# Performance work log

Measured on AMD Instinct MI355X. Metric: run time of the kernel, lower is better.

## Reference

```python
import jax, jax.numpy as jnp
import numpy as np

NEURON_CDECAY = 0.5
NEURON_VDECAY = 0.75
NEURON_VTH = 0.5
SPIKE_WINDOW = 0.5


@jax.custom_vjp
def pseudo_spike(v):
    return (v > NEURON_VTH).astype(v.dtype)

def _ps_fwd(v):
    return pseudo_spike(v), v

def _ps_bwd(v, g):
    return (g * (jnp.abs(v - NEURON_VTH) < SPIKE_WINDOW).astype(g.dtype),)

pseudo_spike.defvjp(_ps_fwd, _ps_bwd)


def setup_inputs() -> dict:
    key = jax.random.key(0)
    ks = jax.random.split(key, 6)
    B, S, T, H, A = 4096, 256, 50, 256, 2
    # NCP mask with fanout=256 over 256 targets selects every target -> dense.
    x = jax.random.uniform(ks[0], (B, S, T), dtype=jnp.float32)
    w1 = jax.random.normal(ks[1], (S, H), dtype=jnp.float32)
    w2 = jax.random.normal(ks[2], (H, H), dtype=jnp.float32)
    w3 = jax.random.normal(ks[3], (H, H), dtype=jnp.float32)
    w4 = jax.random.normal(ks[4], (H, A), dtype=jnp.float32)
    b1 = jnp.zeros((H,), jnp.float32)
    b2 = jnp.zeros((H,), jnp.float32)
    b3 = jnp.zeros((H,), jnp.float32)
    b4 = jnp.zeros((A,), jnp.float32)
    return {"x": x, "w1": w1, "b1": b1, "w2": w2, "b2": b2,
            "w3": w3, "b3": b3, "w4": w4, "b4": b4, "batch_size": B}


def _lif(pre, W, b, u, v, s):
    # torch: linear(pre, weight=W.t(), bias=b) == pre @ W + b  (W is [src, tgt])
    cur = u * NEURON_CDECAY + pre @ W + b
    volt = v * NEURON_VDECAY * (1.0 - s) + cur
    spk = pseudo_spike(volt)
    return cur, volt, spk


def reference(x, w1, b1, w2, b2, w3, b3, w4, b4, batch_size):
    B = x.shape[0]
    T = x.shape[2]
    H1, H2, H3, A = w1.shape[1], w2.shape[1], w3.shape[1], w4.shape[1]
    z = lambda d: jnp.zeros((B, d), x.dtype)
    carry0 = (z(H1), z(H1), z(H1), z(H2), z(H2), z(H2),
              z(H3), z(H3), z(H3), z(A), z(A), z(A))
    xt = jnp.transpose(x, (2, 0, 1))  # [T, B, S]

    def step(carry, inp):
        u1, v1, s1, u2, v2, s2, u3, v3, s3, u4, v4, s4 = carry
        u1, v1, s1 = _lif(inp, w1, b1, u1, v1, s1)
        u2, v2, s2 = _lif(s1, w2, b2, u2, v2, s2)
        u3, v3, s3 = _lif(s2, w3, b3, u3, v3, s3)
        u4, v4, s4 = _lif(s3, w4, b4, u4, v4, s4)
        return (u1, v1, s1, u2, v2, s2, u3, v3, s3, u4, v4, s4), s4

    _, s4_all = jax.lax.scan(step, carry0, xt)  # [T, B, A]
    fc4_sumspike = jnp.sum(s4_all, axis=0) / T
    # faithful to the source: out is divided by batch_window a second time
    out = fc4_sumspike / T
    return out
```

## Files before the change

### kernel.cpp

```cpp
#include <hip/hip_runtime.h>

typedef unsigned short u16;
typedef unsigned int u32;

#define B_N 4096
#define S_N 256
#define T_N 50
#define H_N 256

#define W1F 0
#define W2F 65536
#define W3F 131072
#define W4F 196608
#define B1F 197120
#define B2F 197376
#define B3F 197632
#define B4F 197888
#define CVT_N 197890
#define FLAGI 198656

__device__ __forceinline__ float bf2f(u16 h) { return __uint_as_float(((u32)h) << 16); }
__device__ __forceinline__ u16 f2bf(float f) {
  u32 x = __float_as_uint(f);
  return (u16)((x + 0x7fffu + ((x >> 16) & 1u)) >> 16);
}
__device__ __forceinline__ float ld_f(const void* p, size_t i, int isbf) {
  return isbf ? bf2f(((const u16*)p)[i]) : ((const float*)p)[i];
}

__global__ void detect_dtype(const u16* __restrict__ x, int* __restrict__ flag) {
  __shared__ int cnt[256];
  int c = 0;
  for (int i = threadIdx.x; i < 4096; i += 256) c += (x[2 * i] <= 0x3F80u) ? 1 : 0;
  cnt[threadIdx.x] = c;
  __syncthreads();
  if (threadIdx.x == 0) {
    int tot = 0;
    for (int i = 0; i < 256; i++) tot += cnt[i];
    flag[0] = (tot > 3000) ? 1 : 0;
  }
}

__global__ void convert_inputs(const void* w1, const void* w2, const void* w3,
                               const void* w4, const void* b1, const void* b2,
                               const void* b3, const void* b4, float* __restrict__ ws) {
  const int isbf = ((const int*)ws)[FLAGI];
  int i = blockIdx.x * 256 + threadIdx.x;
  if (i >= CVT_N) return;
  float v;
  if (i < 196608) {
    const void* src = (i < 65536) ? w1 : (i < 131072 ? w2 : w3);
    v = ld_f(src, (size_t)(i & 65535), isbf);
  } else if (i < 197120) v = ld_f(w4, (size_t)(i - W4F), isbf);
  else if (i < 197376) v = ld_f(b1, (size_t)(i - B1F), isbf);
  else if (i < 197632) v = ld_f(b2, (size_t)(i - B2F), isbf);
  else if (i < 197888) v = ld_f(b3, (size_t)(i - B3F), isbf);
  else v = ld_f(b4, (size_t)(i - B4F), isbf);
  ws[i] = v;
}

template <int OFF, int TN>
__device__ __forceinline__ void gemm_win(const float* __restrict__ Wc,
                                         const float (*__restrict__ A)[52],
                                         int rdf, float (&acc)[13][4]) {
  for (int s = 0; s < S_N; s++) {
    const float w0 = Wc[(s << 8) + 0];
    const float w1 = Wc[(s << 8) + 64];
    const float w2 = Wc[(s << 8) + 128];
    const float w3 = Wc[(s << 8) + 192];
    const float4* ar = (const float4*)(&A[s][rdf]);
    const float4 q0 = ar[0], q1 = ar[1], q2 = ar[2], q3 = ar[3];
    const float a[16] = {q0.x, q0.y, q0.z, q0.w, q1.x, q1.y, q1.z, q1.w,
                         q2.x, q2.y, q2.z, q2.w, q3.x, q3.y, q3.z, q3.w};
#pragma unroll
    for (int i = 0; i < TN; i++) {
      acc[i][0] = fmaf(a[OFF + i], w0, acc[i][0]);
      acc[i][1] = fmaf(a[OFF + i], w1, acc[i][1]);
      acc[i][2] = fmaf(a[OFF + i], w2, acc[i][2]);
      acc[i][3] = fmaf(a[OFF + i], w3, acc[i][3]);
    }
  }
}

__global__ __launch_bounds__(256, 3) void snn_f32(
    const void* __restrict__ x, const float* __restrict__ ws, void* __restrict__ out) {
  __shared__ float Af[S_N][52];
  __shared__ float z4[T_N][2];

  const int b = blockIdx.x;
  const int tid = threadIdx.x;
  const int isbf = ((const int*)ws)[FLAGI];
  const int tq = tid >> 6;
  const int hp = tid & 63;
  const int t0 = (tq < 2) ? 13 * tq : 26 + 12 * (tq - 2);
  const int tn = (tq < 2) ? 13 : 12;
  const int rdf = 12 * tq;

  {
    const size_t base = ((size_t)b * S_N + tid) * T_N;
    if (isbf) {
      const u32* xr = (const u32*)((const u16*)x + base);
#pragma unroll
      for (int j = 0; j < 25; j++) {
        u32 d = xr[j];
        Af[tid][2 * j] = bf2f((u16)(d & 0xffffu));
        Af[tid][2 * j + 1] = bf2f((u16)(d >> 16));
      }
    } else {
      const float* xf = (const float*)x + base;
#pragma unroll
      for (int j = 0; j < 25; j++) {
        float2 d = *(const float2*)(xf + 2 * j);
        Af[tid][2 * j] = d.x;
        Af[tid][2 * j + 1] = d.y;
      }
    }
  }

  const int WOFF[3] = {W1F, W2F, W3F};
  const int BOFF[3] = {B1F, B2F, B3F};

  for (int l = 0; l < 3; l++) {
    __syncthreads();
    const float* Wc = ws + WOFF[l] + hp;

    float acc[13][4];
#pragma unroll
    for (int i = 0; i < 13; i++) {
#pragma unroll
      for (int k = 0; k < 4; k++) acc[i][k] = 0.0f;
    }

    if (tq == 0)      gemm_win<0, 13>(Wc, Af, rdf, acc);
    else if (tq == 1) gemm_win<1, 13>(Wc, Af, rdf, acc);
    else              gemm_win<2, 12>(Wc, Af, rdf, acc);
    __syncthreads();

#pragma unroll
    for (int i = 0; i < 13; i++) {
      if (i < tn) {
#pragma unroll
        for (int k = 0; k < 4; k++) Af[hp + 64 * k][t0 + i] = acc[i][k];
      }
    }
    __syncthreads();

    {
      const float bh = ws[BOFF[l] + tid];
      float c[T_N];
      {
        const float4* rr = (const float4*)&Af[tid][0];
#pragma unroll
        for (int j = 0; j < 12; j++) {
          float4 v = rr[j];
          c[4 * j] = v.x; c[4 * j + 1] = v.y; c[4 * j + 2] = v.z; c[4 * j + 3] = v.w;
        }
        float2 v = *(const float2*)&Af[tid][48];
        c[48] = v.x; c[49] = v.y;
      }
      float uu = 0.f, vv = 0.f, ss = 0.f;
#pragma unroll
      for (int t = 0; t < T_N; t++) {
        float cur = fmaf(uu, 0.5f, c[t]) + bh;
        float t1 = vv * 0.75f;
        float volt = fmaf(t1, 1.0f - ss, cur);
        float sp = (volt > 0.5f) ? 1.0f : 0.0f;
        uu = cur; vv = volt; ss = sp;
        c[t] = sp;
      }
      {
        float4* wr = (float4*)&Af[tid][0];
#pragma unroll
        for (int j = 0; j < 12; j++)
          wr[j] = make_float4(c[4 * j], c[4 * j + 1], c[4 * j + 2], c[4 * j + 3]);
        *(float2*)&Af[tid][48] = make_float2(c[48], c[49]);
      }
    }
  }

  __syncthreads();
  if (tid < 2 * T_N) {
    const int t = tid >> 1, a = tid & 1;
    float az = 0.f;
    const float* w4p = ws + W4F + a;
    for (int h = 0; h < H_N; h++) az = fmaf(Af[h][t], w4p[2 * h], az);
    z4[t][a] = az;
  }
  __syncthreads();
  if (tid < 2) {
    const float bh = ws[B4F + tid];
    float uu = 0.f, vv = 0.f, ss = 0.f, sum = 0.f;
    for (int t = 0; t < T_N; t++) {
      float cur = fmaf(uu, 0.5f, z4[t][tid]) + bh;
      float t1 = vv * 0.75f;
      float volt = fmaf(t1, 1.0f - ss, cur);
      float sp = (volt > 0.5f) ? 1.0f : 0.0f;
      uu = cur; vv = volt; ss = sp;
      sum += sp;
    }
    float o = sum / 50.0f / 50.0f;
    if (isbf) ((u16*)out)[b * 2 + tid] = f2bf(o);
    else ((float*)out)[b * 2 + tid] = o;
  }
}

extern "C" void kernel_launch(void* const* d_in, const int* in_sizes, int n_in,
                              void* d_out, int out_size, void* d_ws, size_t ws_size,
                              hipStream_t stream) {
  const void* x  = d_in[0];
  const void* w1 = d_in[1];
  const void* b1 = d_in[2];
  const void* w2 = d_in[3];
  const void* b2 = d_in[4];
  const void* w3 = d_in[5];
  const void* b3 = d_in[6];
  const void* w4 = d_in[7];
  const void* b4 = d_in[8];

  float* ws = (float*)d_ws;
  int* flag = (int*)d_ws + FLAGI;

  detect_dtype<<<1, 256, 0, stream>>>((const u16*)x, flag);
  convert_inputs<<<(CVT_N + 255) / 256, 256, 0, stream>>>(w1, w2, w3, w4, b1, b2, b3, b4, ws);
  snn_f32<<<B_N, 256, 0, stream>>>(x, ws, d_out);
}
```

Measured before the change: 1.178 ms.

## Pack spikes as bitmasks and replace spike GEMMs with masked adds

Layers 2 and 3 now store the LIF spike output as two 32-bit bitmasks per neuron. The GEMM becomes a conditional accumulation of weight rows, with the mask read via readfirstlane since every lane in a wave shares the same timestep mask. Weights are reordered in the convert kernel so each thread fetches its four outputs as one float4. The A-row and weight loads are software-prefetched one step ahead. The intent is to cut FMA work and LDS traffic for binary inputs, at the cost of per-bit branch and select overhead.

```diff
diff --git a/kernel.cpp b/kernel.cpp
--- a/kernel.cpp
+++ b/kernel.cpp
@@ -50,7 +50,9 @@
   float v;
   if (i < 196608) {
     const void* src = (i < 65536) ? w1 : (i < 131072 ? w2 : w3);
-    v = ld_f(src, (size_t)(i & 65535), isbf);
+    const int j = i & 65535;
+    const int k = j & 3, hp = (j >> 2) & 63, s = j >> 8;
+    v = ld_f(src, (size_t)((s << 8) + (k << 6) + hp), isbf);
   } else if (i < 197120) v = ld_f(w4, (size_t)(i - W4F), isbf);
   else if (i < 197376) v = ld_f(b1, (size_t)(i - B1F), isbf);
   else if (i < 197632) v = ld_f(b2, (size_t)(i - B2F), isbf);
@@ -60,26 +62,80 @@
 }
 
 template <int OFF, int TN>
-__device__ __forceinline__ void gemm_win(const float* __restrict__ Wc,
-                                         const float (*__restrict__ A)[52],
-                                         int rdf, float (&acc)[13][4]) {
+__device__ __forceinline__ void gemm_l1(const float4* __restrict__ wp,
+                                        const float (*__restrict__ A)[52],
+                                        int rdf, float (&acc)[13][4]) {
+  const float4* ar0 = (const float4*)(&A[0][rdf]);
+  float4 q0 = ar0[0], q1 = ar0[1], q2 = ar0[2], q3 = ar0[3];
+  float4 wv = wp[0];
   for (int s = 0; s < S_N; s++) {
-    const float w0 = Wc[(s << 8) + 0];
-    const float w1 = Wc[(s << 8) + 64];
-    const float w2 = Wc[(s << 8) + 128];
-    const float w3 = Wc[(s << 8) + 192];
-    const float4* ar = (const float4*)(&A[s][rdf]);
-    const float4 q0 = ar[0], q1 = ar[1], q2 = ar[2], q3 = ar[3];
+    const int sn = (s + 1) & 255;
+    const float4* arn = (const float4*)(&A[sn][rdf]);
+    float4 p0 = arn[0], p1 = arn[1], p2 = arn[2], p3 = arn[3];
+    float4 wn = wp[(size_t)sn << 6];
     const float a[16] = {q0.x, q0.y, q0.z, q0.w, q1.x, q1.y, q1.z, q1.w,
                          q2.x, q2.y, q2.z, q2.w, q3.x, q3.y, q3.z, q3.w};
 #pragma unroll
     for (int i = 0; i < TN; i++) {
-      acc[i][0] = fmaf(a[OFF + i], w0, acc[i][0]);
-      acc[i][1] = fmaf(a[OFF + i], w1, acc[i][1]);
-      acc[i][2] = fmaf(a[OFF + i], w2, acc[i][2]);
-      acc[i][3] = fmaf(a[OFF + i], w3, acc[i][3]);
-    }
-  }
+      acc[i][0] = fmaf(a[OFF + i], wv.x, acc[i][0]);
+      acc[i][1] = fmaf(a[OFF + i], wv.y, acc[i][1]);
+      acc[i][2] = fmaf(a[OFF + i], wv.z, acc[i][2]);
+      acc[i][3] = fmaf(a[OFF + i], wv.w, acc[i][3]);
+    }
+    q0 = p0; q1 = p1; q2 = p2; q3 = p3; wv = wn;
+  }
+}
+
+template <int T0, int TN>
+__device__ __forceinline__ void gemm_sp(const float4* __restrict__ wp,
+                                        const float (*__restrict__ A)[52],
+                                        float (&acc)[13][4]) {
+  uint2 bv = *(const uint2*)(&A[0][50]);
+  float4 wv = wp[0];
+  for (int s = 0; s < S_N; s++) {
+    const int sn = (s + 1) & 255;
+    uint2 bn = *(const uint2*)(&A[sn][50]);
+    float4 wn = wp[(size_t)sn << 6];
+    const u32 bw0 = (u32)__builtin_amdgcn_readfirstlane((int)bv.x);
+    const u32 bw1 = (u32)__builtin_amdgcn_readfirstlane((int)bv.y);
+#pragma unroll
+    for (int i = 0; i < TN; i++) {
+      const int t = T0 + i;
+      const u32 bw = (t < 32) ? bw0 : bw1;
+      if (bw & (1u << (t & 31))) {
+        acc[i][0] += wv.x; acc[i][1] += wv.y; acc[i][2] += wv.z; acc[i][3] += wv.w;
+      }
+    }
+    bv = bn; wv = wn;
+  }
+}
+
+__device__ __forceinline__ void lif_scan(float (*Af)[52], int tid, float bh) {
+  float c[T_N];
+  {
+    const float4* rr = (const float4*)&Af[tid][0];
+#pragma unroll
+    for (int j = 0; j < 12; j++) {
+      float4 v = rr[j];
+      c[4 * j] = v.x; c[4 * j + 1] = v.y; c[4 * j + 2] = v.z; c[4 * j + 3] = v.w;
+    }
+    float2 v = *(const float2*)&Af[tid][48];
+    c[48] = v.x; c[49] = v.y;
+  }
+  float uu = 0.f, vv = 0.f, ss = 0.f;
+  u32 bw0 = 0u, bw1 = 0u;
+#pragma unroll
+  for (int t = 0; t < T_N; t++) {
+    float cur = fmaf(uu, 0.5f, c[t]) + bh;
+    float t1 = vv * 0.75f;
+    float volt = fmaf(t1, 1.0f - ss, cur);
+    bool sp = volt > 0.5f;
+    if (t < 32) bw0 |= sp ? (1u << t) : 0u;
+    else        bw1 |= sp ? (1u << (t - 32)) : 0u;
+    uu = cur; vv = volt; ss = sp ? 1.0f : 0.0f;
+  }
+  ((u32*)&Af[tid][50])[0] = bw0;
+  ((u32*)&Af[tid][50])[1] = bw1;
 }
 
 __global__ __launch_bounds__(256, 3) void snn_f32(
@@ -122,7 +178,7 @@
 
   for (int l = 0; l < 3; l++) {
     __syncthreads();
-    const float* Wc = ws + WOFF[l] + hp;
+    const float4* wp = (const float4*)(ws + WOFF[l]) + hp;
 
     float acc[13][4];
 #pragma unroll
@@ -131,9 +187,17 @@
       for (int k = 0; k < 4; k++) acc[i][k] = 0.0f;
     }
 
-    if (tq == 0)      gemm_win<0, 13>(Wc, Af, rdf, acc);
-    else if (tq == 1) gemm_win<1, 13>(Wc, Af, rdf, acc);
-    else              gemm_win<2, 12>(Wc, Af, rdf, acc);
+    if (l == 0) {
+      if (tq == 0)      gemm_l1<0, 13>(wp, Af, 0, acc);
+      else if (tq == 1) gemm_l1<1, 13>(wp, Af, 12, acc);
+      else if (tq == 2) gemm_l1<2, 12>(wp, Af, 24, acc);
+      else              gemm_l1<2, 12>(wp, Af, 36, acc);
+    } else {
+      if (tq == 0)      gemm_sp<0, 13>(wp, Af, acc);
+      else if (tq == 1) gemm_sp<13, 13>(wp, Af, acc);
+      else if (tq == 2) gemm_sp<26, 12>(wp, Af, acc);
+      else              gemm_sp<38, 12>(wp, Af, acc);
+    }
     __syncthreads();
 
 #pragma unroll
@@ -145,45 +209,20 @@
     }
     __syncthreads();
 
-    {
-      const float bh = ws[BOFF[l] + tid];
-      float c[T_N];
-      {
-        const float4* rr = (const float4*)&Af[tid][0];
-#pragma unroll
-        for (int j = 0; j < 12; j++) {
-          float4 v = rr[j];
-          c[4 * j] = v.x; c[4 * j + 1] = v.y; c[4 * j + 2] = v.z; c[4 * j + 3] = v.w;
-        }
-        float2 v = *(const float2*)&Af[tid][48];
-        c[48] = v.x; c[49] = v.y;
-      }
-      float uu = 0.f, vv = 0.f, ss = 0.f;
-#pragma unroll
-      for (int t = 0; t < T_N; t++) {
-        float cur = fmaf(uu, 0.5f, c[t]) + bh;
-        float t1 = vv * 0.75f;
-        float volt = fmaf(t1, 1.0f - ss, cur);
-        float sp = (volt > 0.5f) ? 1.0f : 0.0f;
-        uu = cur; vv = volt; ss = sp;
-        c[t] = sp;
-      }
-      {
-        float4* wr = (float4*)&Af[tid][0];
-#pragma unroll
-        for (int j = 0; j < 12; j++)
-          wr[j] = make_float4(c[4 * j], c[4 * j + 1], c[4 * j + 2], c[4 * j + 3]);
-        *(float2*)&Af[tid][48] = make_float2(c[48], c[49]);
-      }
-    }
+    lif_scan(Af, tid, ws[BOFF[l] + tid]);
   }
 
   __syncthreads();
   if (tid < 2 * T_N) {
     const int t = tid >> 1, a = tid & 1;
+    const int wd = t >> 5, bt = t & 31;
     float az = 0.f;
     const float* w4p = ws + W4F + a;
-    for (int h = 0; h < H_N; h++) az = fmaf(Af[h][t], w4p[2 * h], az);
+    for (int h = 0; h < H_N; h++) {
+      const u32 bits = ((const u32*)&Af[h][50])[wd];
+      const float m = (float)((bits >> bt) & 1u);
+      az = fmaf(m, w4p[2 * h], az);
+    }
     z4[t][a] = az;
   }
   __syncthreads();
```

After: 1.268 ms. 1.08x slower.
